# Kernel optimization log

Hardware: AMD Instinct MI355X
Metric: run time of the kernel (lower is better)

The kernel has to match this reference:

```python
import jax, jax.numpy as jnp
import numpy as np

D, H, HKV, HD = 1024, 16, 4, 64
ROPE_BASE = 10000.0
QK_GAIN_INIT = 1.0


def setup_inputs() -> dict:
    key = jax.random.key(0)
    ks = jax.random.split(key, 6)
    B, S = 2, 2048
    kv_dim = HKV * HD
    x = jax.random.normal(ks[0], (B, S, D), dtype=jnp.float32)
    Wq = jax.random.normal(ks[1], (D, D), dtype=jnp.float32) * 0.02
    Wk = jax.random.normal(ks[2], (kv_dim, D), dtype=jnp.float32) * 0.02
    Wv = jax.random.normal(ks[3], (kv_dim, D), dtype=jnp.float32) * 0.02
    Wo = jax.random.normal(ks[4], (D, D), dtype=jnp.float32) * 0.02
    q_gain = jnp.full((H,), QK_GAIN_INIT, dtype=jnp.float32)
    return {"x": x, "Wq": Wq, "Wk": Wk, "Wv": Wv, "Wo": Wo, "q_gain": q_gain}


def _rms_norm(t):
    eps = jnp.finfo(t.dtype).eps
    return t * jax.lax.rsqrt(jnp.mean(t * t, axis=-1, keepdims=True) + eps)


def _rope(t, cos, sin):
    # t: [B,h,S,HD]; cos/sin: [1,1,S,HD//2]
    half = t.shape[-1] // 2
    t1, t2 = t[..., :half], t[..., half:]
    return jnp.concatenate((t1 * cos + t2 * sin, -t1 * sin + t2 * cos), axis=-1)


def _attention(x, Wq, Wk, Wv, Wo, q_gain):
    B, S, _ = x.shape
    q = (x @ Wq.T).reshape(B, S, H, HD).transpose(0, 2, 1, 3)     # [B,H,S,HD]
    k = (x @ Wk.T).reshape(B, S, HKV, HD).transpose(0, 2, 1, 3)   # [B,HKV,S,HD]
    v = (x @ Wv.T).reshape(B, S, HKV, HD).transpose(0, 2, 1, 3)
    q, k = _rms_norm(q), _rms_norm(k)
    # rotary tables
    inv_freq = 1.0 / (ROPE_BASE ** (jnp.arange(0, HD, 2, dtype=jnp.float32) / HD))
    freqs = jnp.arange(S, dtype=jnp.float32)[:, None] * inv_freq[None, :]  # [S,HD//2]
    cos, sin = jnp.cos(freqs)[None, None], jnp.sin(freqs)[None, None]
    q, k = _rope(q, cos, sin), _rope(k, cos, sin)
    q = q * q_gain[None, :, None, None]
    # GQA: repeat kv heads to match query heads
    g = H // HKV
    k = jnp.repeat(k, g, axis=1)
    v = jnp.repeat(v, g, axis=1)
    scale = 1.0 / jnp.sqrt(jnp.asarray(HD, q.dtype))
    scores = jnp.einsum('bhqd,bhkd->bhqk', q, k) * scale
    causal = jnp.tril(jnp.ones((S, S), dtype=bool))
    scores = jnp.where(causal[None, None], scores, jnp.asarray(-jnp.inf, scores.dtype))
    attn = jax.nn.softmax(scores, axis=-1)
    y = jnp.einsum('bhqk,bhkd->bhqd', attn, v)                    # [B,H,S,HD]
    y = y.transpose(0, 2, 1, 3).reshape(B, S, D)
    return y @ Wo.T


def reference(x, Wq, Wk, Wv, Wo, q_gain):
    return _attention(x, Wq, Wk, Wv, Wo, q_gain)
```

## Files before the change

kernel.cpp:

```cpp
#include <hip/hip_runtime.h>
#include <hip/hip_bf16.h>
#include <math.h>

typedef __attribute__((ext_vector_type(8))) __bf16 bf16x8;
typedef __attribute__((ext_vector_type(4))) short short4v;
typedef __attribute__((ext_vector_type(4))) float f32x4;
typedef __attribute__((ext_vector_type(4))) unsigned short ushort4v;
typedef __attribute__((ext_vector_type(8))) unsigned short ushort8;

#define LOG2E 1.44269504088896340736f

static __device__ __forceinline__ unsigned short f2bf(float f) {
  unsigned int u = __float_as_uint(f);
  return (unsigned short)((u + 0x7fffu + ((u >> 16) & 1u)) >> 16);
}
static __device__ __forceinline__ short bfbits(float f) {
  __bf16 h = (__bf16)f;
  return __builtin_bit_cast(short, h);
}
static __device__ __forceinline__ float bf2f(unsigned short u) {
  unsigned int v = ((unsigned int)u) << 16;
  return __builtin_bit_cast(float, v);
}

static __device__ __forceinline__ void gload16(const unsigned short* g, void* l) {
  __builtin_amdgcn_global_load_lds(
      (const __attribute__((address_space(1))) unsigned int*)g,
      (__attribute__((address_space(3))) unsigned int*)l, 16, 0, 0);
}

__global__ __launch_bounds__(256) void prep_kernel(
    const float* __restrict__ x, const float* __restrict__ Wq,
    const float* __restrict__ Wk, const float* __restrict__ Wv,
    const float* __restrict__ Wo,
    unsigned short* __restrict__ xb, unsigned short* __restrict__ wqkv,
    unsigned short* __restrict__ wo_b, float* __restrict__ tab) {
  const int bx = blockIdx.x, tid = threadIdx.x;
  if (bx < 6656) {
    const float* src;
    unsigned short* dst;
    int i;
    if (bx < 4096)       { src = x;  dst = xb;             i = bx * 256 + tid; }
    else if (bx < 5120)  { src = Wq; dst = wqkv;           i = (bx - 4096) * 256 + tid; }
    else if (bx < 5376)  { src = Wk; dst = wqkv + 1048576; i = (bx - 5120) * 256 + tid; }
    else if (bx < 5632)  { src = Wv; dst = wqkv + 1310720; i = (bx - 5376) * 256 + tid; }
    else                 { src = Wo; dst = wo_b;           i = (bx - 5632) * 256 + tid; }
    float4 v = reinterpret_cast<const float4*>(src)[i];
    ushort4v o;
    o.x = f2bf(v.x); o.y = f2bf(v.y); o.z = f2bf(v.z); o.w = f2bf(v.w);
    reinterpret_cast<ushort4v*>(dst)[i] = o;
  } else {
    int i = (bx - 6656) * 256 + tid;
    int s = i >> 5, d = i & 31;
    float invf = powf(10000.f, -(float)d / 32.f);
    float fr = (float)s * invf;
    tab[s * 64 + d] = cosf(fr);
    tab[s * 64 + 32 + d] = sinf(fr);
  }
}

template <bool B16OUT>
__global__ __launch_bounds__(256) void gemm_bt_kernel(
    const unsigned short* __restrict__ A, const unsigned short* __restrict__ B,
    void* __restrict__ Cv, int M, int N, int K, int nbn) {
  __shared__ unsigned short sA[64 * 64];
  __shared__ unsigned short sB[128 * 64];
  const int t = threadIdx.x;
  const int lane = t & 63;
  const int w = t >> 6;
  const int bm = blockIdx.x / nbn, bn = blockIdx.x % nbn;
  const long m0 = (long)bm * 64, n0 = (long)bn * 128;
  const int wm = (w >> 1) * 32, wn = (w & 1) * 64;
  const int lr = lane & 15, lg = lane >> 4;
  f32x4 acc[2][4];
#pragma unroll
  for (int i = 0; i < 2; i++)
#pragma unroll
    for (int j = 0; j < 4; j++) acc[i][j] = (f32x4){0.f, 0.f, 0.f, 0.f};

  for (int k0 = 0; k0 < K; k0 += 64) {
#pragma unroll
    for (int i = 0; i < 2; i++) {
      int chunk = i * 256 + t;
      int r = chunk >> 3;
      int c = (chunk & 7) << 3;
      gload16(A + (m0 + r) * (long)K + k0 + c, (char*)sA + chunk * 16);
    }
#pragma unroll
    for (int i = 0; i < 4; i++) {
      int chunk = i * 256 + t;
      int r = chunk >> 3;
      int c = (chunk & 7) << 3;
      gload16(B + (n0 + r) * (long)K + k0 + c, (char*)sB + chunk * 16);
    }
    __syncthreads();
#pragma unroll
    for (int kk = 0; kk < 2; ++kk) {
      bf16x8 af[2], bfr[4];
#pragma unroll
      for (int m = 0; m < 2; m++)
        af[m] = *(const bf16x8*)&sA[(wm + m * 16 + lr) * 64 + kk * 32 + lg * 8];
#pragma unroll
      for (int n = 0; n < 4; n++)
        bfr[n] = *(const bf16x8*)&sB[(wn + n * 16 + lr) * 64 + kk * 32 + lg * 8];
#pragma unroll
      for (int m = 0; m < 2; m++)
#pragma unroll
        for (int n = 0; n < 4; n++)
          acc[m][n] = __builtin_amdgcn_mfma_f32_16x16x32_bf16(af[m], bfr[n], acc[m][n], 0, 0, 0);
    }
    __syncthreads();
  }
#pragma unroll
  for (int m = 0; m < 2; m++) {
#pragma unroll
    for (int n = 0; n < 4; n++) {
      long col = n0 + wn + n * 16 + lr;
#pragma unroll
      for (int j = 0; j < 4; j++) {
        long row = m0 + wm + m * 16 + lg * 4 + j;
        if (B16OUT)
          ((unsigned short*)Cv)[row * N + col] = f2bf(acc[m][n][j]);
        else
          ((float*)Cv)[row * N + col] = acc[m][n][j];
      }
    }
  }
}

__global__ __launch_bounds__(256) void pack_kernel(
    const unsigned short* __restrict__ qkv, const float* __restrict__ tab,
    const float* __restrict__ qg,
    unsigned short* __restrict__ qb, unsigned short* __restrict__ kb) {
  const int wid = (blockIdx.x * 256 + threadIdx.x) >> 6;
  const int lane = threadIdx.x & 63;
  const int row = wid / 20;
  const int u = wid % 20;
  const int b = row >> 11, s = row & 2047;
  float v;
  if (u < 16) v = bf2f(qkv[(size_t)row * 1536 + u * 64 + lane]);
  else        v = bf2f(qkv[(size_t)row * 1536 + 1024 + (u - 16) * 64 + lane]);
  float ss = v * v;
#pragma unroll
  for (int m = 32; m >= 1; m >>= 1) ss += __shfl_xor(ss, m);
  float n = v * rsqrtf(ss * (1.0f / 64.0f) + 1.1920929e-07f);
  int i = lane & 31;
  float c = tab[s * 64 + i], sn = tab[s * 64 + 32 + i];
  float p = __shfl_xor(n, 32);
  float o = (lane < 32) ? (n * c + p * sn) : (n * c - p * sn);
  if (u < 16) {
    o *= qg[u] * (0.125f * LOG2E);
    qb[((size_t)(b * 16 + u) * 2048 + s) * 64 + lane] = f2bf(o);
  } else {
    kb[((size_t)(b * 4 + (u - 16)) * 2048 + s) * 64 + lane] = f2bf(o);
  }
}

__global__ __launch_bounds__(256) void vpack_kernel(
    const unsigned short* __restrict__ qkv, unsigned short* __restrict__ vtb) {
  __shared__ unsigned short sT[64 * 65];
  const int tid = threadIdx.x;
  const int bhk = blockIdx.x >> 5;
  const int st = blockIdx.x & 31;
  const int b = bhk >> 2, hk = bhk & 3;
  const int r = tid >> 2, cg = (tid & 3) << 4;
  const unsigned short* src = qkv + (size_t)(b * 2048 + st * 64 + r) * 1536 + 1280 + hk * 64 + cg;
  ushort8 v0 = *(const ushort8*)src;
  ushort8 v1 = *(const ushort8*)(src + 8);
#pragma unroll
  for (int k = 0; k < 8; ++k) sT[r * 65 + cg + k] = v0[k];
#pragma unroll
  for (int k = 0; k < 8; ++k) sT[r * 65 + cg + 8 + k] = v1[k];
  __syncthreads();
  const int d = tid >> 2, sg = (tid & 3) << 4;
  ushort8 o0, o1;
#pragma unroll
  for (int k = 0; k < 8; ++k) o0[k] = sT[(sg + k) * 65 + d];
#pragma unroll
  for (int k = 0; k < 8; ++k) o1[k] = sT[(sg + 8 + k) * 65 + d];
  unsigned short* dst = vtb + ((size_t)(bhk * 64 + d)) * 2048 + st * 64 + sg;
  *(ushort8*)dst = o0;
  *(ushort8*)(dst + 8) = o1;
}

__global__ __launch_bounds__(256) void attn_kernel(
    const unsigned short* __restrict__ qb, const unsigned short* __restrict__ kb,
    const unsigned short* __restrict__ vtb, unsigned short* __restrict__ yb,
    const float* __restrict__ qg) {
  __shared__ unsigned short sK[2][64 * 64];
  __shared__ unsigned short sV[2][64 * 64];
  const int tid = threadIdx.x;
  const int lane = tid & 63;
  const int w = tid >> 6;
  const int qt = 31 - (blockIdx.x >> 5);
  const int bh = blockIdx.x & 31;
  const int h = bh & 15;
  const int b = bh >> 4;
  const float M = 11.7f * fabsf(qg[h]);
  const int q0 = qt * 64 + w * 16;
  const unsigned short* Q  = qb  + (size_t)(b * 16 + h) * 2048 * 64;
  const unsigned short* Kp = kb  + (size_t)(b * 4 + (h >> 2)) * 2048 * 64;
  const unsigned short* Vp = vtb + (size_t)(b * 4 + (h >> 2)) * 64 * 2048;
  const int qc = lane & 15;
  const int g = lane >> 4;
  const int qrow = q0 + qc;
  const bf16x8 qf0 = *(const bf16x8*)(Q + (size_t)qrow * 64 + g * 8);
  const bf16x8 qf1 = *(const bf16x8*)(Q + (size_t)qrow * 64 + 32 + g * 8);
  f32x4 acc[4];
  acc[0] = acc[1] = acc[2] = acc[3] = (f32x4){0.f, 0.f, 0.f, 0.f};
  float lsum = 0.f;
  const int nt = qt + 1;

  const int r0 = tid >> 3, c0 = tid & 7;
  const int swz = ((c0 ^ (r0 & 7)) << 3);
  const unsigned short* gK = Kp + (size_t)r0 * 64 + swz;
  const unsigned short* gV = Vp + (size_t)r0 * 2048 + swz;

  gload16(gK,             (char*)&sK[0][0] + tid * 16);
  gload16(gK + 32 * 64,   (char*)&sK[0][0] + (tid + 256) * 16);
  gload16(gV,             (char*)&sV[0][0] + tid * 16);
  gload16(gV + 32 * 2048, (char*)&sV[0][0] + (tid + 256) * 16);
  gK += 64 * 64; gV += 64;

  int cur = 0;
  for (int t = 0; t < nt; ++t) {
    __syncthreads();
    if (t + 1 < nt) {
      const int nb = cur ^ 1;
      gload16(gK,             (char*)&sK[nb][0] + tid * 16);
      gload16(gK + 32 * 64,   (char*)&sK[nb][0] + (tid + 256) * 16);
      gload16(gV,             (char*)&sV[nb][0] + tid * 16);
      gload16(gV + 32 * 2048, (char*)&sV[nb][0] + (tid + 256) * 16);
      gK += 64 * 64; gV += 64;
    }
    const unsigned short* sKc = &sK[cur][0];
    const unsigned short* sVc = &sV[cur][0];
    f32x4 st[4];
    __builtin_amdgcn_s_setprio(1);
#pragma unroll
    for (int ks = 0; ks < 4; ++ks) {
      const int rr = ks * 16 + qc;
      bf16x8 kf0 = *(const bf16x8*)&sKc[rr * 64 + ((g ^ (rr & 7)) << 3)];
      bf16x8 kf1 = *(const bf16x8*)&sKc[rr * 64 + (((4 + g) ^ (rr & 7)) << 3)];
      f32x4 a = (f32x4){0.f, 0.f, 0.f, 0.f};
      a = __builtin_amdgcn_mfma_f32_16x16x32_bf16(kf0, qf0, a, 0, 0, 0);
      a = __builtin_amdgcn_mfma_f32_16x16x32_bf16(kf1, qf1, a, 0, 0, 0);
      st[ks] = a;
    }
    __builtin_amdgcn_s_setprio(0);
    if (t == nt - 1) {
#pragma unroll
      for (int ks = 0; ks < 4; ++ks)
#pragma unroll
        for (int j = 0; j < 4; ++j)
          if (ks * 16 + g * 4 + j > w * 16 + qc) st[ks][j] = -1e30f;
    }
    short4v pb[4];
#pragma unroll
    for (int ks = 0; ks < 4; ++ks)
#pragma unroll
      for (int j = 0; j < 4; ++j) {
        float p = exp2f(st[ks][j] - M);
        lsum += p;
        pb[ks][j] = bfbits(p);
      }
    __builtin_amdgcn_s_setprio(1);
#pragma unroll
    for (int ks = 0; ks < 4; ++ks) {
#pragma unroll
      for (int d = 0; d < 4; ++d) {
        const int rd = d * 16 + qc;
        const int el = rd * 64 + ((((ks * 2 + (g >> 1)) ^ (rd & 7)) << 3) + ((g & 1) << 2));
        short4v vf = *(const short4v*)&sVc[el];
        acc[d] = __builtin_amdgcn_mfma_f32_16x16x16bf16_1k(vf, pb[ks], acc[d], 0, 0, 0);
      }
    }
    __builtin_amdgcn_s_setprio(0);
    cur ^= 1;
  }
  float l = lsum;
  l += __shfl_xor(l, 16);
  l += __shfl_xor(l, 32);
  const float inv = 1.0f / l;
  unsigned short* Y = yb + (size_t)(b * 2048 + qrow) * 1024 + h * 64;
#pragma unroll
  for (int d = 0; d < 4; ++d)
#pragma unroll
    for (int j = 0; j < 4; ++j)
      Y[d * 16 + g * 4 + j] = (unsigned short)bfbits(acc[d][j] * inv);
}

extern "C" void kernel_launch(void* const* d_in, const int* in_sizes, int n_in,
                              void* d_out, int out_size, void* d_ws, size_t ws_size,
                              hipStream_t stream) {
  const float* x  = (const float*)d_in[0];
  const float* Wq = (const float*)d_in[1];
  const float* Wk = (const float*)d_in[2];
  const float* Wv = (const float*)d_in[3];
  const float* Wo = (const float*)d_in[4];
  const float* qg = (const float*)d_in[5];
  float* out = (float*)d_out;

  char* ws = (char*)d_ws;
  const size_t NEED = 47710208;
  if (ws_size < NEED) return;
  unsigned short* xb   = (unsigned short*)(ws);
  unsigned short* wqkv = (unsigned short*)(ws + 8388608);
  unsigned short* wo_b = (unsigned short*)(ws + 11534336);
  unsigned short* qkvb = (unsigned short*)(ws + 13631488);
  unsigned short* qbuf = (unsigned short*)(ws + 26214400);
  unsigned short* kbuf = (unsigned short*)(ws + 34603008);
  unsigned short* vtb  = (unsigned short*)(ws + 36700160);
  unsigned short* ybuf = (unsigned short*)(ws + 38797312);
  float*          tab  = (float*)        (ws + 47185920);

  prep_kernel<<<6912, 256, 0, stream>>>(x, Wq, Wk, Wv, Wo, xb, wqkv, wo_b, tab);
  gemm_bt_kernel<true><<<64 * 12, 256, 0, stream>>>(xb, wqkv, qkvb, 4096, 1536, 1024, 12);
  pack_kernel<<<20480, 256, 0, stream>>>(qkvb, tab, qg, qbuf, kbuf);
  vpack_kernel<<<256, 256, 0, stream>>>(qkvb, vtb);
  attn_kernel<<<1024, 256, 0, stream>>>(qbuf, kbuf, vtb, ybuf, qg);
  gemm_bt_kernel<false><<<64 * 8, 256, 0, stream>>>(ybuf, wo_b, out, 4096, 1024, 1024, 8);
}
```

Baseline: 119.7 us.

## Process 128 query rows per attention block to reuse K/V tiles

Each attention block now covers 128 query rows instead of 64. Each wave handles two 16-row query subtiles against every K/V tile staged in shared memory, which halves global and LDS K/V traffic per query and gives more MFMAs per LDS read. The grid shrinks to 512 blocks and the causal loop walks twice as many 64-key tiles per block, masking the last two. The cost is more registers per wave, fewer blocks to spread across CUs, and coarser load balancing under the causal triangle.

```diff
diff --git a/kernel.cpp b/kernel.cpp
--- a/kernel.cpp
+++ b/kernel.cpp
@@ -192,24 +192,31 @@
   const int tid = threadIdx.x;
   const int lane = tid & 63;
   const int w = tid >> 6;
-  const int qt = 31 - (blockIdx.x >> 5);
+  const int qt = 15 - (blockIdx.x >> 5);
   const int bh = blockIdx.x & 31;
   const int h = bh & 15;
   const int b = bh >> 4;
   const float M = 11.7f * fabsf(qg[h]);
-  const int q0 = qt * 64 + w * 16;
+  const int q0 = qt * 128 + w * 32;
   const unsigned short* Q  = qb  + (size_t)(b * 16 + h) * 2048 * 64;
   const unsigned short* Kp = kb  + (size_t)(b * 4 + (h >> 2)) * 2048 * 64;
   const unsigned short* Vp = vtb + (size_t)(b * 4 + (h >> 2)) * 64 * 2048;
   const int qc = lane & 15;
   const int g = lane >> 4;
-  const int qrow = q0 + qc;
-  const bf16x8 qf0 = *(const bf16x8*)(Q + (size_t)qrow * 64 + g * 8);
-  const bf16x8 qf1 = *(const bf16x8*)(Q + (size_t)qrow * 64 + 32 + g * 8);
-  f32x4 acc[4];
-  acc[0] = acc[1] = acc[2] = acc[3] = (f32x4){0.f, 0.f, 0.f, 0.f};
-  float lsum = 0.f;
-  const int nt = qt + 1;
+  bf16x8 qf[2][2];
+#pragma unroll
+  for (int qi = 0; qi < 2; ++qi) {
+    const size_t qr = (size_t)(q0 + qi * 16 + qc) * 64;
+    qf[qi][0] = *(const bf16x8*)(Q + qr + g * 8);
+    qf[qi][1] = *(const bf16x8*)(Q + qr + 32 + g * 8);
+  }
+  f32x4 acc[2][4];
+#pragma unroll
+  for (int qi = 0; qi < 2; ++qi)
+#pragma unroll
+    for (int d = 0; d < 4; ++d) acc[qi][d] = (f32x4){0.f, 0.f, 0.f, 0.f};
+  float lsum[2] = {0.f, 0.f};
+  const int ntb = 2 * qt + 2;
 
   const int r0 = tid >> 3, c0 = tid & 7;
   const int swz = ((c0 ^ (r0 & 7)) << 3);
@@ -223,9 +230,9 @@
   gK += 64 * 64; gV += 64;
 
   int cur = 0;
-  for (int t = 0; t < nt; ++t) {
+  for (int t = 0; t < ntb; ++t) {
     __syncthreads();
-    if (t + 1 < nt) {
+    if (t + 1 < ntb) {
       const int nb = cur ^ 1;
       gload16(gK,             (char*)&sK[nb][0] + tid * 16);
       gload16(gK + 32 * 64,   (char*)&sK[nb][0] + (tid + 256) * 16);
@@ -235,35 +242,39 @@
     }
     const unsigned short* sKc = &sK[cur][0];
     const unsigned short* sVc = &sV[cur][0];
-    f32x4 st[4];
-    __builtin_amdgcn_s_setprio(1);
-#pragma unroll
-    for (int ks = 0; ks < 4; ++ks) {
-      const int rr = ks * 16 + qc;
-      bf16x8 kf0 = *(const bf16x8*)&sKc[rr * 64 + ((g ^ (rr & 7)) << 3)];
-      bf16x8 kf1 = *(const bf16x8*)&sKc[rr * 64 + (((4 + g) ^ (rr & 7)) << 3)];
-      f32x4 a = (f32x4){0.f, 0.f, 0.f, 0.f};
-      a = __builtin_amdgcn_mfma_f32_16x16x32_bf16(kf0, qf0, a, 0, 0, 0);
-      a = __builtin_amdgcn_mfma_f32_16x16x32_bf16(kf1, qf1, a, 0, 0, 0);
-      st[ks] = a;
-    }
-    __builtin_amdgcn_s_setprio(0);
-    if (t == nt - 1) {
+    short4v pb[2][4];
+#pragma unroll
+    for (int qi = 0; qi < 2; ++qi) {
+      f32x4 st[4];
+      __builtin_amdgcn_s_setprio(1);
+#pragma unroll
+      for (int ks = 0; ks < 4; ++ks) {
+        const int rr = ks * 16 + qc;
+        bf16x8 kf0 = *(const bf16x8*)&sKc[rr * 64 + ((g ^ (rr & 7)) << 3)];
+        bf16x8 kf1 = *(const bf16x8*)&sKc[rr * 64 + (((4 + g) ^ (rr & 7)) << 3)];
+        f32x4 a = (f32x4){0.f, 0.f, 0.f, 0.f};
+        a = __builtin_amdgcn_mfma_f32_16x16x32_bf16(kf0, qf[qi][0], a, 0, 0, 0);
+        a = __builtin_amdgcn_mfma_f32_16x16x32_bf16(kf1, qf[qi][1], a, 0, 0, 0);
+        st[ks] = a;
+      }
+      __builtin_amdgcn_s_setprio(0);
+      if (t >= ntb - 2) {
+        const int qrow = q0 + qi * 16 + qc;
+#pragma unroll
+        for (int ks = 0; ks < 4; ++ks)
+#pragma unroll
+          for (int j = 0; j < 4; ++j)
+            if ((t << 6) + ks * 16 + g * 4 + j > qrow) st[ks][j] = -1e30f;
+      }
 #pragma unroll
       for (int ks = 0; ks < 4; ++ks)
 #pragma unroll
-        for (int j = 0; j < 4; ++j)
-          if (ks * 16 + g * 4 + j > w * 16 + qc) st[ks][j] = -1e30f;
-    }
-    short4v pb[4];
-#pragma unroll
-    for (int ks = 0; ks < 4; ++ks)
-#pragma unroll
-      for (int j = 0; j < 4; ++j) {
-        float p = exp2f(st[ks][j] - M);
-        lsum += p;
-        pb[ks][j] = bfbits(p);
-      }
+        for (int j = 0; j < 4; ++j) {
+          float p = exp2f(st[ks][j] - M);
+          lsum[qi] += p;
+          pb[qi][ks][j] = bfbits(p);
+        }
+    }
     __builtin_amdgcn_s_setprio(1);
 #pragma unroll
     for (int ks = 0; ks < 4; ++ks) {
@@ -272,22 +283,26 @@
         const int rd = d * 16 + qc;
         const int el = rd * 64 + ((((ks * 2 + (g >> 1)) ^ (rd & 7)) << 3) + ((g & 1) << 2));
         short4v vf = *(const short4v*)&sVc[el];
-        acc[d] = __builtin_amdgcn_mfma_f32_16x16x16bf16_1k(vf, pb[ks], acc[d], 0, 0, 0);
+        acc[0][d] = __builtin_amdgcn_mfma_f32_16x16x16bf16_1k(vf, pb[0][ks], acc[0][d], 0, 0, 0);
+        acc[1][d] = __builtin_amdgcn_mfma_f32_16x16x16bf16_1k(vf, pb[1][ks], acc[1][d], 0, 0, 0);
       }
     }
     __builtin_amdgcn_s_setprio(0);
     cur ^= 1;
   }
-  float l = lsum;
-  l += __shfl_xor(l, 16);
-  l += __shfl_xor(l, 32);
-  const float inv = 1.0f / l;
-  unsigned short* Y = yb + (size_t)(b * 2048 + qrow) * 1024 + h * 64;
-#pragma unroll
-  for (int d = 0; d < 4; ++d)
-#pragma unroll
-    for (int j = 0; j < 4; ++j)
-      Y[d * 16 + g * 4 + j] = (unsigned short)bfbits(acc[d][j] * inv);
+#pragma unroll
+  for (int qi = 0; qi < 2; ++qi) {
+    float l = lsum[qi];
+    l += __shfl_xor(l, 16);
+    l += __shfl_xor(l, 32);
+    const float inv = 1.0f / l;
+    unsigned short* Y = yb + (size_t)(b * 2048 + q0 + qi * 16 + qc) * 1024 + h * 64;
+#pragma unroll
+    for (int d = 0; d < 4; ++d)
+#pragma unroll
+      for (int j = 0; j < 4; ++j)
+        Y[d * 16 + g * 4 + j] = (unsigned short)bfbits(acc[qi][d][j] * inv);
+  }
 }
 
 extern "C" void kernel_launch(void* const* d_in, const int* in_sizes, int n_in,
@@ -318,6 +333,6 @@
   gemm_bt_kernel<true><<<64 * 12, 256, 0, stream>>>(xb, wqkv, qkvb, 4096, 1536, 1024, 12);
   pack_kernel<<<20480, 256, 0, stream>>>(qkvb, tab, qg, qbuf, kbuf);
   vpack_kernel<<<256, 256, 0, stream>>>(qkvb, vtb);
-  attn_kernel<<<1024, 256, 0, stream>>>(qbuf, kbuf, vtb, ybuf, qg);
+  attn_kernel<<<512, 256, 0, stream>>>(qbuf, kbuf, vtb, ybuf, qg);
   gemm_bt_kernel<false><<<64 * 8, 256, 0, stream>>>(ybuf, wo_b, out, 4096, 1024, 1024, 8);
 }
```

After: 138.9 us. +16.0%, slower.

## Split long causal query tiles across two blocks and combine partial sums

Applied to the files above, without the earlier changes.

For the 16 longest query tiles per head, the key range is split into two halves processed by separate blocks, which write unnormalized fp32 partial accumulators and row sums to workspace. A new combine kernel adds the halves, normalizes and writes bf16 output. This targets the tail imbalance of causal attention, where the longest tiles dominate the kernel's critical path. The cost is a 1536-block grid, an extra launch, and fp32 partial traffic. The workspace layout is reshuffled so the partials overlay the x buffer, which is dead by then.

```diff
diff --git a/kernel.cpp b/kernel.cpp
--- a/kernel.cpp
+++ b/kernel.cpp
@@ -186,16 +186,21 @@
 __global__ __launch_bounds__(256) void attn_kernel(
     const unsigned short* __restrict__ qb, const unsigned short* __restrict__ kb,
     const unsigned short* __restrict__ vtb, unsigned short* __restrict__ yb,
-    const float* __restrict__ qg) {
+    const float* __restrict__ qg, float* __restrict__ pacc,
+    float* __restrict__ plsum) {
   __shared__ unsigned short sK[2][64 * 64];
   __shared__ unsigned short sV[2][64 * 64];
   const int tid = threadIdx.x;
   const int lane = tid & 63;
   const int w = tid >> 6;
-  const int qt = 31 - (blockIdx.x >> 5);
+  const int u = blockIdx.x >> 5;
   const int bh = blockIdx.x & 31;
   const int h = bh & 15;
   const int b = bh >> 4;
+  int qt, t0, t1, half;
+  if (u < 16)      { qt = 31 - u; half = 0; t0 = 0;             t1 = (qt + 1) >> 1; }
+  else if (u < 32) { qt = 47 - u; half = 1; t0 = (qt + 1) >> 1; t1 = qt + 1; }
+  else             { qt = 47 - u; half = 2; t0 = 0;             t1 = qt + 1; }
   const float M = 11.7f * fabsf(qg[h]);
   const int q0 = qt * 64 + w * 16;
   const unsigned short* Q  = qb  + (size_t)(b * 16 + h) * 2048 * 64;
@@ -209,12 +214,11 @@
   f32x4 acc[4];
   acc[0] = acc[1] = acc[2] = acc[3] = (f32x4){0.f, 0.f, 0.f, 0.f};
   float lsum = 0.f;
-  const int nt = qt + 1;
 
   const int r0 = tid >> 3, c0 = tid & 7;
   const int swz = ((c0 ^ (r0 & 7)) << 3);
-  const unsigned short* gK = Kp + (size_t)r0 * 64 + swz;
-  const unsigned short* gV = Vp + (size_t)r0 * 2048 + swz;
+  const unsigned short* gK = Kp + (size_t)(t0 * 64 + r0) * 64 + swz;
+  const unsigned short* gV = Vp + (size_t)r0 * 2048 + t0 * 64 + swz;
 
   gload16(gK,             (char*)&sK[0][0] + tid * 16);
   gload16(gK + 32 * 64,   (char*)&sK[0][0] + (tid + 256) * 16);
@@ -223,9 +227,9 @@
   gK += 64 * 64; gV += 64;
 
   int cur = 0;
-  for (int t = 0; t < nt; ++t) {
+  for (int t = t0; t < t1; ++t) {
     __syncthreads();
-    if (t + 1 < nt) {
+    if (t + 1 < t1) {
       const int nb = cur ^ 1;
       gload16(gK,             (char*)&sK[nb][0] + tid * 16);
       gload16(gK + 32 * 64,   (char*)&sK[nb][0] + (tid + 256) * 16);
@@ -248,12 +252,12 @@
       st[ks] = a;
     }
     __builtin_amdgcn_s_setprio(0);
-    if (t == nt - 1) {
+    if (t == qt) {
 #pragma unroll
       for (int ks = 0; ks < 4; ++ks)
 #pragma unroll
         for (int j = 0; j < 4; ++j)
-          if (ks * 16 + g * 4 + j > w * 16 + qc) st[ks][j] = -1e30f;
+          if ((t << 6) + ks * 16 + g * 4 + j > qrow) st[ks][j] = -1e30f;
     }
     short4v pb[4];
 #pragma unroll
@@ -281,13 +285,42 @@
   float l = lsum;
   l += __shfl_xor(l, 16);
   l += __shfl_xor(l, 32);
-  const float inv = 1.0f / l;
-  unsigned short* Y = yb + (size_t)(b * 2048 + qrow) * 1024 + h * 64;
-#pragma unroll
-  for (int d = 0; d < 4; ++d)
-#pragma unroll
-    for (int j = 0; j < 4; ++j)
-      Y[d * 16 + g * 4 + j] = (unsigned short)bfbits(acc[d][j] * inv);
+  if (half == 2) {
+    const float inv = 1.0f / l;
+    unsigned short* Y = yb + (size_t)(b * 2048 + qrow) * 1024 + h * 64;
+#pragma unroll
+    for (int d = 0; d < 4; ++d)
+#pragma unroll
+      for (int j = 0; j < 4; ++j)
+        Y[d * 16 + g * 4 + j] = (unsigned short)bfbits(acc[d][j] * inv);
+  } else {
+    const int lrow = w * 16 + qc;
+    const size_t base = ((size_t)(bh * 2 + half) * 16 + (qt - 16));
+    float* pa = pacc + base * 4096 + lrow * 64;
+#pragma unroll
+    for (int d = 0; d < 4; ++d)
+#pragma unroll
+      for (int j = 0; j < 4; ++j)
+        pa[d * 16 + g * 4 + j] = acc[d][j];
+    if (g == 0) plsum[base * 64 + lrow] = l;
+  }
+}
+
+__global__ __launch_bounds__(256) void combine_kernel(
+    const float* __restrict__ pacc, const float* __restrict__ plsum,
+    unsigned short* __restrict__ yb) {
+  const int e = blockIdx.x * 256 + threadIdx.x;
+  const int d = e & 63;
+  const int lrow = (e >> 6) & 63;
+  const int qx = (e >> 12) & 15;
+  const int bh = e >> 16;
+  const int b = bh >> 4, h = bh & 15;
+  const size_t iA = ((size_t)(bh * 2 + 0) * 16 + qx) * 4096 + lrow * 64 + d;
+  const size_t iB = ((size_t)(bh * 2 + 1) * 16 + qx) * 4096 + lrow * 64 + d;
+  const float l = plsum[((bh * 2 + 0) * 16 + qx) * 64 + lrow] +
+                  plsum[((bh * 2 + 1) * 16 + qx) * 64 + lrow];
+  const float y = (pacc[iA] + pacc[iB]) / l;
+  yb[((size_t)(b * 2048 + (16 + qx) * 64 + lrow)) * 1024 + h * 64 + d] = f2bf(y);
 }
 
 extern "C" void kernel_launch(void* const* d_in, const int* in_sizes, int n_in,
@@ -306,18 +339,21 @@
   if (ws_size < NEED) return;
   unsigned short* xb   = (unsigned short*)(ws);
   unsigned short* wqkv = (unsigned short*)(ws + 8388608);
-  unsigned short* wo_b = (unsigned short*)(ws + 11534336);
-  unsigned short* qkvb = (unsigned short*)(ws + 13631488);
-  unsigned short* qbuf = (unsigned short*)(ws + 26214400);
-  unsigned short* kbuf = (unsigned short*)(ws + 34603008);
-  unsigned short* vtb  = (unsigned short*)(ws + 36700160);
-  unsigned short* ybuf = (unsigned short*)(ws + 38797312);
-  float*          tab  = (float*)        (ws + 47185920);
+  unsigned short* qkvb = (unsigned short*)(ws + 11534336);
+  unsigned short* qbuf = (unsigned short*)(ws + 24117248);
+  unsigned short* kbuf = (unsigned short*)(ws + 32505856);
+  unsigned short* vtb  = (unsigned short*)(ws + 34603008);
+  unsigned short* ybuf = (unsigned short*)(ws + 36700160);
+  float*          tab  = (float*)        (ws + 45088768);
+  unsigned short* wo_b = (unsigned short*)(ws + 45613056);
+  float* pacc  = (float*)(ws);
+  float* plsum = (float*)(ws + 16777216);
 
   prep_kernel<<<6912, 256, 0, stream>>>(x, Wq, Wk, Wv, Wo, xb, wqkv, wo_b, tab);
   gemm_bt_kernel<true><<<64 * 12, 256, 0, stream>>>(xb, wqkv, qkvb, 4096, 1536, 1024, 12);
   pack_kernel<<<20480, 256, 0, stream>>>(qkvb, tab, qg, qbuf, kbuf);
   vpack_kernel<<<256, 256, 0, stream>>>(qkvb, vtb);
-  attn_kernel<<<1024, 256, 0, stream>>>(qbuf, kbuf, vtb, ybuf, qg);
+  attn_kernel<<<1536, 256, 0, stream>>>(qbuf, kbuf, vtb, ybuf, qg, pacc, plsum);
+  combine_kernel<<<8192, 256, 0, stream>>>(pacc, plsum, ybuf);
   gemm_bt_kernel<false><<<64 * 8, 256, 0, stream>>>(ybuf, wo_b, out, 4096, 1024, 1024, 8);
 }
```

Measured after the change: 125.3 us. 4.7% more time.

## Switch attention to 32x32x16 MFMA with two 32-row waves per block

Applied to the files above, without the earlier changes.

Rewrites the attention kernel so each block uses two waves of 32 query rows and performs QK^T and PV with 32x32x16 bf16 MFMA instead of 16x16 MFMAs. The probability tile is packed to bf16 with v_cvt_pk_bf16_f32 and rearranged across half-waves with v_permlane32_swap, so it can feed the PV MFMA directly. Tile staging is spread across 128 threads with more loads each. The aim is fewer MFMA issues and less LDS fragment traffic per FLOP, at the cost of lower thread count per block and higher register pressure.

```diff
diff --git a/kernel.cpp b/kernel.cpp
--- a/kernel.cpp
+++ b/kernel.cpp
@@ -5,8 +5,10 @@
 typedef __attribute__((ext_vector_type(8))) __bf16 bf16x8;
 typedef __attribute__((ext_vector_type(4))) short short4v;
 typedef __attribute__((ext_vector_type(4))) float f32x4;
+typedef __attribute__((ext_vector_type(16))) float f32x16;
 typedef __attribute__((ext_vector_type(4))) unsigned short ushort4v;
 typedef __attribute__((ext_vector_type(8))) unsigned short ushort8;
+typedef __attribute__((ext_vector_type(4))) unsigned int uint4v;
 
 #define LOG2E 1.44269504088896340736f
 
@@ -183,7 +185,7 @@
   *(ushort8*)(dst + 8) = o1;
 }
 
-__global__ __launch_bounds__(256) void attn_kernel(
+__global__ __launch_bounds__(128) void attn_kernel(
     const unsigned short* __restrict__ qb, const unsigned short* __restrict__ kb,
     const unsigned short* __restrict__ vtb, unsigned short* __restrict__ yb,
     const float* __restrict__ qg) {
@@ -197,17 +199,19 @@
   const int h = bh & 15;
   const int b = bh >> 4;
   const float M = 11.7f * fabsf(qg[h]);
-  const int q0 = qt * 64 + w * 16;
+  const int q0 = qt * 64 + w * 32;
   const unsigned short* Q  = qb  + (size_t)(b * 16 + h) * 2048 * 64;
   const unsigned short* Kp = kb  + (size_t)(b * 4 + (h >> 2)) * 2048 * 64;
   const unsigned short* Vp = vtb + (size_t)(b * 4 + (h >> 2)) * 64 * 2048;
-  const int qc = lane & 15;
-  const int g = lane >> 4;
-  const int qrow = q0 + qc;
-  const bf16x8 qf0 = *(const bf16x8*)(Q + (size_t)qrow * 64 + g * 8);
-  const bf16x8 qf1 = *(const bf16x8*)(Q + (size_t)qrow * 64 + 32 + g * 8);
-  f32x4 acc[4];
-  acc[0] = acc[1] = acc[2] = acc[3] = (f32x4){0.f, 0.f, 0.f, 0.f};
+  const int ql = lane & 31;
+  const int hh = lane >> 5;
+  bf16x8 qf[4];
+#pragma unroll
+  for (int dsl = 0; dsl < 4; ++dsl)
+    qf[dsl] = *(const bf16x8*)(Q + (size_t)(q0 + ql) * 64 + dsl * 16 + hh * 8);
+  f32x16 acc[2];
+#pragma unroll
+  for (int e = 0; e < 16; ++e) { acc[0][e] = 0.f; acc[1][e] = 0.f; }
   float lsum = 0.f;
   const int nt = qt + 1;
 
@@ -216,78 +220,106 @@
   const unsigned short* gK = Kp + (size_t)r0 * 64 + swz;
   const unsigned short* gV = Vp + (size_t)r0 * 2048 + swz;
 
-  gload16(gK,             (char*)&sK[0][0] + tid * 16);
-  gload16(gK + 32 * 64,   (char*)&sK[0][0] + (tid + 256) * 16);
-  gload16(gV,             (char*)&sV[0][0] + tid * 16);
-  gload16(gV + 32 * 2048, (char*)&sV[0][0] + (tid + 256) * 16);
+#define STAGE_TILE(bufi)                                              \
+  do {                                                                \
+    gload16(gK,             (char*)&sK[bufi][0] + tid * 16);          \
+    gload16(gK + 16 * 64,   (char*)&sK[bufi][0] + (tid + 128) * 16);  \
+    gload16(gK + 32 * 64,   (char*)&sK[bufi][0] + (tid + 256) * 16);  \
+    gload16(gK + 48 * 64,   (char*)&sK[bufi][0] + (tid + 384) * 16);  \
+    gload16(gV,             (char*)&sV[bufi][0] + tid * 16);          \
+    gload16(gV + 16 * 2048, (char*)&sV[bufi][0] + (tid + 128) * 16);  \
+    gload16(gV + 32 * 2048, (char*)&sV[bufi][0] + (tid + 256) * 16);  \
+    gload16(gV + 48 * 2048, (char*)&sV[bufi][0] + (tid + 384) * 16);  \
+  } while (0)
+
+  STAGE_TILE(0);
   gK += 64 * 64; gV += 64;
 
   int cur = 0;
   for (int t = 0; t < nt; ++t) {
     __syncthreads();
     if (t + 1 < nt) {
-      const int nb = cur ^ 1;
-      gload16(gK,             (char*)&sK[nb][0] + tid * 16);
-      gload16(gK + 32 * 64,   (char*)&sK[nb][0] + (tid + 256) * 16);
-      gload16(gV,             (char*)&sV[nb][0] + tid * 16);
-      gload16(gV + 32 * 2048, (char*)&sV[nb][0] + (tid + 256) * 16);
+      STAGE_TILE(cur ^ 1);
       gK += 64 * 64; gV += 64;
     }
     const unsigned short* sKc = &sK[cur][0];
     const unsigned short* sVc = &sV[cur][0];
-    f32x4 st[4];
+    f32x16 st[2];
     __builtin_amdgcn_s_setprio(1);
 #pragma unroll
-    for (int ks = 0; ks < 4; ++ks) {
-      const int rr = ks * 16 + qc;
-      bf16x8 kf0 = *(const bf16x8*)&sKc[rr * 64 + ((g ^ (rr & 7)) << 3)];
-      bf16x8 kf1 = *(const bf16x8*)&sKc[rr * 64 + (((4 + g) ^ (rr & 7)) << 3)];
-      f32x4 a = (f32x4){0.f, 0.f, 0.f, 0.f};
-      a = __builtin_amdgcn_mfma_f32_16x16x32_bf16(kf0, qf0, a, 0, 0, 0);
-      a = __builtin_amdgcn_mfma_f32_16x16x32_bf16(kf1, qf1, a, 0, 0, 0);
-      st[ks] = a;
+    for (int kvt = 0; kvt < 2; ++kvt) {
+      const int row = kvt * 32 + ql;
+      f32x16 a;
+#pragma unroll
+      for (int e = 0; e < 16; ++e) a[e] = 0.f;
+#pragma unroll
+      for (int dsl = 0; dsl < 4; ++dsl) {
+        const int ch = dsl * 2 + hh;
+        bf16x8 kf = *(const bf16x8*)&sKc[row * 64 + ((ch ^ (row & 7)) << 3)];
+        a = __builtin_amdgcn_mfma_f32_32x32x16_bf16(kf, qf[dsl], a, 0, 0, 0);
+      }
+      st[kvt] = a;
     }
     __builtin_amdgcn_s_setprio(0);
     if (t == nt - 1) {
 #pragma unroll
-      for (int ks = 0; ks < 4; ++ks)
-#pragma unroll
-        for (int j = 0; j < 4; ++j)
-          if (ks * 16 + g * 4 + j > w * 16 + qc) st[ks][j] = -1e30f;
-    }
-    short4v pb[4];
-#pragma unroll
-    for (int ks = 0; ks < 4; ++ks)
-#pragma unroll
-      for (int j = 0; j < 4; ++j) {
-        float p = exp2f(st[ks][j] - M);
-        lsum += p;
-        pb[ks][j] = bfbits(p);
+      for (int kvt = 0; kvt < 2; ++kvt)
+#pragma unroll
+        for (int r = 0; r < 16; ++r) {
+          const int kvl = kvt * 32 + (r & 3) + 8 * (r >> 2) + 4 * hh;
+          if (kvl > w * 32 + ql) st[kvt][r] = -1e30f;
+        }
+    }
+    bf16x8 pb[4];
+#pragma unroll
+    for (int kvt = 0; kvt < 2; ++kvt) {
+      float p[16];
+#pragma unroll
+      for (int r = 0; r < 16; ++r) {
+        p[r] = exp2f(st[kvt][r] - M);
+        lsum += p[r];
       }
+      unsigned int X[8];
+#pragma unroll
+      for (int i = 0; i < 8; ++i)
+        asm("v_cvt_pk_bf16_f32 %0, %1, %2" : "=v"(X[i]) : "v"(p[2 * i]), "v"(p[2 * i + 1]));
+      asm("v_permlane32_swap_b32 %0, %1" : "+v"(X[0]), "+v"(X[2]));
+      asm("v_permlane32_swap_b32 %0, %1" : "+v"(X[1]), "+v"(X[3]));
+      asm("v_permlane32_swap_b32 %0, %1" : "+v"(X[4]), "+v"(X[6]));
+      asm("v_permlane32_swap_b32 %0, %1" : "+v"(X[5]), "+v"(X[7]));
+      uint4v u0 = {X[0], X[1], X[2], X[3]};
+      uint4v u1 = {X[4], X[5], X[6], X[7]};
+      pb[2 * kvt]     = __builtin_bit_cast(bf16x8, u0);
+      pb[2 * kvt + 1] = __builtin_bit_cast(bf16x8, u1);
+    }
     __builtin_amdgcn_s_setprio(1);
 #pragma unroll
     for (int ks = 0; ks < 4; ++ks) {
 #pragma unroll
-      for (int d = 0; d < 4; ++d) {
-        const int rd = d * 16 + qc;
-        const int el = rd * 64 + ((((ks * 2 + (g >> 1)) ^ (rd & 7)) << 3) + ((g & 1) << 2));
-        short4v vf = *(const short4v*)&sVc[el];
-        acc[d] = __builtin_amdgcn_mfma_f32_16x16x16bf16_1k(vf, pb[ks], acc[d], 0, 0, 0);
+      for (int dt = 0; dt < 2; ++dt) {
+        const int row = dt * 32 + ql;
+        const int ch = ks * 2 + hh;
+        bf16x8 vf = *(const bf16x8*)&sVc[row * 64 + ((ch ^ (row & 7)) << 3)];
+        acc[dt] = __builtin_amdgcn_mfma_f32_32x32x16_bf16(vf, pb[ks], acc[dt], 0, 0, 0);
       }
     }
     __builtin_amdgcn_s_setprio(0);
     cur ^= 1;
   }
-  float l = lsum;
-  l += __shfl_xor(l, 16);
-  l += __shfl_xor(l, 32);
-  const float inv = 1.0f / l;
-  unsigned short* Y = yb + (size_t)(b * 2048 + qrow) * 1024 + h * 64;
-#pragma unroll
-  for (int d = 0; d < 4; ++d)
-#pragma unroll
-    for (int j = 0; j < 4; ++j)
-      Y[d * 16 + g * 4 + j] = (unsigned short)bfbits(acc[d][j] * inv);
+#undef STAGE_TILE
+  lsum += __shfl_xor(lsum, 32);
+  const float inv = 1.0f / lsum;
+  unsigned short* Y = yb + (size_t)(b * 2048 + q0 + ql) * 1024 + h * 64;
+#pragma unroll
+  for (int dt = 0; dt < 2; ++dt) {
+#pragma unroll
+    for (int rg = 0; rg < 4; ++rg) {
+      ushort4v o;
+#pragma unroll
+      for (int j = 0; j < 4; ++j) o[j] = f2bf(acc[dt][rg * 4 + j] * inv);
+      *(ushort4v*)(Y + dt * 32 + rg * 8 + hh * 4) = o;
+    }
+  }
 }
 
 extern "C" void kernel_launch(void* const* d_in, const int* in_sizes, int n_in,
@@ -318,6 +350,6 @@
   gemm_bt_kernel<true><<<64 * 12, 256, 0, stream>>>(xb, wqkv, qkvb, 4096, 1536, 1024, 12);
   pack_kernel<<<20480, 256, 0, stream>>>(qkvb, tab, qg, qbuf, kbuf);
   vpack_kernel<<<256, 256, 0, stream>>>(qkvb, vtb);
-  attn_kernel<<<1024, 256, 0, stream>>>(qbuf, kbuf, vtb, ybuf, qg);
+  attn_kernel<<<1024, 128, 0, stream>>>(qbuf, kbuf, vtb, ybuf, qg);
   gemm_bt_kernel<false><<<64 * 8, 256, 0, stream>>>(ybuf, wo_b, out, 4096, 1024, 1024, 8);
 }
```

Measured after the change: 140.7 us. +17.5%, slower.
